# Optimization experiments

Measured on AMD Instinct MI355X. Metric: run time of the kernel, lower is better.

Reference implementation:

```python
import jax, jax.numpy as jnp
import numpy as np

H_PATCH = 32
W_PATCH = 32
DIM = 512
HEADS = 8
DIM_HEAD = 64
INNER = HEADS * DIM_HEAD
N = H_PATCH * W_PATCH
BATCH = 32


def make_relative_position_index(h, w):
    coords = np.stack(np.meshgrid(np.arange(h), np.arange(w), indexing='ij'))  # [2,h,w]
    flat = coords.reshape(2, -1)  # [2, N]
    rel = flat[:, :, None] - flat[:, None, :]  # [2, N, N]
    rel = rel.transpose(1, 2, 0).copy()  # [N, N, 2]
    rel[:, :, 0] += h - 1
    rel[:, :, 1] += w - 1
    rel[:, :, 0] *= 2 * h - 1
    return jnp.asarray(rel.sum(-1), dtype=jnp.int32)  # [N, N]


def setup_inputs() -> dict:
    key = jax.random.key(0)
    k1, k2, k3, k4 = jax.random.split(key, 4)
    x = jax.random.normal(k1, (BATCH, N, DIM), dtype=jnp.float32)
    w_qkv = jax.random.normal(k2, (DIM, 3 * INNER), dtype=jnp.float32) * (DIM ** -0.5)
    w_out = jax.random.normal(k3, (INNER, DIM), dtype=jnp.float32) * (INNER ** -0.5)
    b_out = jnp.zeros((DIM,), dtype=jnp.float32)
    bias_table = jax.random.normal(k4, ((2 * H_PATCH - 1) * (2 * W_PATCH - 1), HEADS), dtype=jnp.float32) * 0.02
    rel_index = make_relative_position_index(H_PATCH, W_PATCH)
    return {"x": x, "w_qkv": w_qkv, "w_out": w_out, "b_out": b_out,
            "bias_table": bias_table, "rel_index": rel_index}


def reference(x, w_qkv, w_out, b_out, bias_table, rel_index):
    b, n, _ = x.shape
    scale = DIM_HEAD ** -0.5
    qkv = x @ w_qkv  # [b, n, 3*inner]
    q, k, v = jnp.split(qkv, 3, axis=-1)
    def heads(t):
        return t.reshape(b, n, HEADS, DIM_HEAD).transpose(0, 2, 1, 3)  # [b,h,n,d]
    q, k, v = heads(q), heads(k), heads(v)
    dots = jnp.einsum('bhnd,bhmd->bhnm', q, k) * scale  # [b,h,n,n]
    bias = bias_table[rel_index]  # [n,n,heads]
    dots = dots + bias.transpose(2, 0, 1)[None]  # [b,h,n,n]
    attn = jax.nn.softmax(dots, axis=-1)
    out = jnp.einsum('bhnm,bhmd->bhnd', attn, v)
    out = out.transpose(0, 2, 1, 3).reshape(b, n, INNER)
    return out @ w_out + b_out
```

## Files before the change

### kernel.cpp

```cpp
#include <hip/hip_runtime.h>
#include <stdint.h>

typedef unsigned short u16;
typedef __attribute__((ext_vector_type(8))) short short8;
typedef __attribute__((ext_vector_type(4))) float floatx4;

__device__ __forceinline__ u16 f2bf(float f) {
  union { float f; unsigned u; } v; v.f = f;
  return (u16)((v.u + 0x7FFFu + ((v.u >> 16) & 1u)) >> 16);
}
__device__ __forceinline__ void gl_lds16(const void* g, void* l) {
  __builtin_amdgcn_global_load_lds((const __attribute__((address_space(1))) void*)g,
                                   (__attribute__((address_space(3))) void*)l, 16, 0, 0);
}
__device__ __forceinline__ float exp2_fast(float x) {
#if __has_builtin(__builtin_amdgcn_exp2f)
  return __builtin_amdgcn_exp2f(x);
#else
  return exp2f(x);
#endif
}

__global__ __launch_bounds__(256) void k_cast_x(const float* __restrict__ x, u16* __restrict__ xb) {
  int t = blockIdx.x * 256 + threadIdx.x;
  const float4* xv = (const float4*)x;
  float4 a = xv[2 * t], b = xv[2 * t + 1];
  short8 o;
  o[0] = f2bf(a.x); o[1] = f2bf(a.y); o[2] = f2bf(a.z); o[3] = f2bf(a.w);
  o[4] = f2bf(b.x); o[5] = f2bf(b.y); o[6] = f2bf(b.z); o[7] = f2bf(b.w);
  ((short8*)xb)[t] = o;
}

__global__ __launch_bounds__(256) void k_prep_w(const float* __restrict__ wqkv, const float* __restrict__ wout,
                                                u16* __restrict__ wqkvT, u16* __restrict__ woutT) {
  int t = blockIdx.x * 256 + threadIdx.x;
  if (t < 786432) {
    int n = t >> 9, k = t & 511;
    wqkvT[t] = f2bf(wqkv[k * 1536 + n]);
  } else {
    int u = t - 786432;
    int n = u >> 9, k = u & 511;
    woutT[u] = f2bf(wout[k * 512 + n]);
  }
}

__global__ __launch_bounds__(256) void k_prep_bias(const int* __restrict__ rel, const float* __restrict__ tab,
                                                   u16* __restrict__ biasb) {
  int t = blockIdx.x * 256 + threadIdx.x;
  int r    = t & 3;
  int ti   = (t >> 2) & 1;
  int l15  = (t >> 3) & 15;
  int quad = (t >> 7) & 3;
  int w    = (t >> 9) & 3;
  int kt   = (t >> 11) & 7;
  int qt   = (t >> 14) & 7;
  int h    = t >> 17;
  int qrow = qt * 128 + w * 32 + ti * 16 + quad * 4 + r;
  const int* rr = rel + qrow * 1024 + kt * 128 + l15;
  short8 o;
  #pragma unroll
  for (int tj = 0; tj < 8; tj++) {
    int idx = rr[tj * 16];
    o[tj] = f2bf((tab[idx * 8 + h] - 8.0f) * 1.44269504f);
  }
  ((short8*)biasb)[t] = o;
}

__global__ __launch_bounds__(256) void k_gemm_qkv(const u16* __restrict__ xb, const u16* __restrict__ wT,
                                                  u16* __restrict__ qbuf, u16* __restrict__ kbuf,
                                                  u16* __restrict__ vtbuf) {
  __shared__ u16 sm[17408];
  const int bn = blockIdx.x, bm = blockIdx.y;
  const int tid = threadIdx.x, w = tid >> 6, lane = tid & 63;
  const int quad = lane >> 4, l15 = lane & 15;
  const int wr = w >> 1, wc = w & 1;
  const u16* Ag = xb + (size_t)bm * 128 * 512;
  const u16* Bg = wT + (size_t)bn * 128 * 512;
  floatx4 acc[4][4];
  floatx4 zero = {0.f, 0.f, 0.f, 0.f};
  #pragma unroll
  for (int i = 0; i < 4; i++)
    #pragma unroll
    for (int j = 0; j < 4; j++) acc[i][j] = zero;

  for (int kb = 0; kb < 512; kb += 32) {
    __syncthreads();
    #pragma unroll
    for (int i = 0; i < 2; i++) {
      int c = w * 128 + i * 64 + lane;
      int row = c >> 2, col = (c & 3) * 8;
      gl_lds16(Ag + (size_t)row * 512 + kb + col, &sm[(w * 128 + i * 64) * 8]);
      gl_lds16(Bg + (size_t)row * 512 + kb + col, &sm[4096 + (w * 128 + i * 64) * 8]);
    }
    __syncthreads();
    short8 af[4], bf[4];
    #pragma unroll
    for (int ti = 0; ti < 4; ti++)
      af[ti] = *(const short8*)&sm[(wr * 64 + ti * 16 + l15) * 32 + quad * 8];
    #pragma unroll
    for (int tj = 0; tj < 4; tj++)
      bf[tj] = *(const short8*)&sm[4096 + (wc * 64 + tj * 16 + l15) * 32 + quad * 8];
    #pragma unroll
    for (int ti = 0; ti < 4; ti++)
      #pragma unroll
      for (int tj = 0; tj < 4; tj++)
        acc[ti][tj] = __builtin_amdgcn_mfma_f32_16x16x32_bf16(af[ti], bf[tj], acc[ti][tj], 0, 0, 0);
  }
  __syncthreads();
  #pragma unroll
  for (int ti = 0; ti < 4; ti++)
    #pragma unroll
    for (int tj = 0; tj < 4; tj++)
      #pragma unroll
      for (int r = 0; r < 4; r++)
        sm[(wr * 64 + ti * 16 + quad * 4 + r) * 136 + wc * 64 + tj * 16 + l15] = f2bf(acc[ti][tj][r]);
  __syncthreads();
  const int b = bm >> 3;
  const int nrow0 = (bm & 7) * 128;
  if (bn < 8) {
    u16* dst = (bn < 4) ? qbuf : kbuf;
    #pragma unroll
    for (int i = 0; i < 8; i++) {
      int chunk = i * 256 + tid;
      int r = chunk >> 4, c8 = chunk & 15;
      int nin = (bn & 3) * 128 + c8 * 8;
      int h = nin >> 6, d = nin & 63;
      uint4 val = *(const uint4*)&sm[r * 136 + c8 * 8];
      *(uint4*)&dst[(((size_t)(b * 8 + h)) * 1024 + nrow0 + r) * 64 + d] = val;
    }
  } else {
    #pragma unroll
    for (int i = 0; i < 8; i++) {
      int chunk = i * 256 + tid;
      int dcol = chunk & 127, nr8 = chunk >> 7;
      int nin = (bn & 3) * 128 + dcol;
      int h = nin >> 6, d = nin & 63;
      short8 v;
      #pragma unroll
      for (int j = 0; j < 8; j++) v[j] = (short)sm[(nr8 * 8 + j) * 136 + dcol];
      *(short8*)&vtbuf[(((size_t)(b * 8 + h)) * 64 + d) * 1024 + nrow0 + nr8 * 8] = v;
    }
  }
}

__global__ __launch_bounds__(256, 2) void k_attn(const u16* __restrict__ qbuf, const u16* __restrict__ kbuf,
                                                 const u16* __restrict__ vtbuf, const u16* __restrict__ biasb,
                                                 u16* __restrict__ attn_out) {
  __shared__ u16 sm[40960];
  const int PO = 32768;
  const int b = blockIdx.x, h = blockIdx.y >> 3, qt = blockIdx.y & 7;
  const int tid = threadIdx.x, w = tid >> 6, lane = tid & 63;
  const int quad = lane >> 4, l15 = lane & 15;
  const int xm = l15 & 7;
  u16* pw = &sm[PO + w * 2048];
  const size_t bh = (size_t)(b * 8 + h);
  const u16* qg = qbuf + (bh * 1024 + (size_t)qt * 128) * 64;
  const u16* kg = kbuf + bh * 1024 * 64;
  const u16* vg = vtbuf + bh * 64 * 1024;
  const u16* bg = biasb + (size_t)h * 1048576 + (size_t)qt * 131072 +
                  (size_t)w * 4096 + quad * 1024 + l15 * 64;

  int rK[4], cK[4], dV[4], cV[4];
  #pragma unroll
  for (int i = 0; i < 4; i++) {
    int p = (w * 4 + i) * 64 + lane;
    rK[i] = p >> 3;  cK[i] = (p & 7) ^ (rK[i] & 7);
    dV[i] = p >> 4;  cV[i] = (p & 15) ^ (dV[i] & 7);
  }

  short8 qf[2][2];
  #pragma unroll
  for (int ti = 0; ti < 2; ti++)
    #pragma unroll
    for (int kk = 0; kk < 2; kk++)
      qf[ti][kk] = *(const short8*)&qg[(w * 32 + ti * 16 + l15) * 64 + kk * 32 + quad * 8];

  floatx4 oacc[2][4];
  floatx4 zero = {0.f, 0.f, 0.f, 0.f};
  #pragma unroll
  for (int i = 0; i < 2; i++)
    #pragma unroll
    for (int j = 0; j < 4; j++) oacc[i][j] = zero;
  float lrow[2][4];
  #pragma unroll
  for (int i = 0; i < 2; i++)
    #pragma unroll
    for (int r = 0; r < 4; r++) lrow[i][r] = 0.f;

  const float SC = 0.125f * 1.44269504f;

  #pragma unroll
  for (int i = 0; i < 4; i++) {
    gl_lds16(kg + (size_t)rK[i] * 64 + cK[i] * 8, &sm[(w * 4 + i) * 512]);
    gl_lds16(vg + (size_t)dV[i] * 1024 + cV[i] * 8, &sm[8192 + (w * 4 + i) * 512]);
  }
  __syncthreads();

  for (int kt = 0; kt < 8; kt++) {
    const int cur = (kt & 1) ? 16384 : 0;
    const int nxt = (kt & 1) ? 0 : 16384;
    if (kt < 7) {
      #pragma unroll
      for (int i = 0; i < 4; i++) {
        gl_lds16(kg + (size_t)((kt + 1) * 128 + rK[i]) * 64 + cK[i] * 8, &sm[nxt + (w * 4 + i) * 512]);
        gl_lds16(vg + (size_t)dV[i] * 1024 + (kt + 1) * 128 + cV[i] * 8, &sm[nxt + 8192 + (w * 4 + i) * 512]);
      }
    }
    const u16* bkt = bg + kt * 16384;
    uint2 bu[2][4][2];
    #pragma unroll
    for (int ti = 0; ti < 2; ti++)
      #pragma unroll
      for (int r = 0; r < 4; r++) {
        bu[ti][r][0] = *(const uint2*)&bkt[(ti * 4 + r) * 8];
        bu[ti][r][1] = *(const uint2*)&bkt[(ti * 4 + r) * 8 + 4];
      }

    #pragma unroll
    for (int tjh = 0; tjh < 2; tjh++) {
      floatx4 sacc[2][4];
      #pragma unroll
      for (int tjl = 0; tjl < 4; tjl++) { sacc[0][tjl] = zero; sacc[1][tjl] = zero; }
      #pragma unroll
      for (int tjl = 0; tjl < 4; tjl++) {
        int tj = tjh * 4 + tjl;
        #pragma unroll
        for (int kk = 0; kk < 2; kk++) {
          short8 kf = *(const short8*)&sm[cur + (tj * 16 + l15) * 64 + ((kk * 4 + quad) ^ xm) * 8];
          sacc[0][tjl] = __builtin_amdgcn_mfma_f32_16x16x32_bf16(qf[0][kk], kf, sacc[0][tjl], 0, 0, 0);
          sacc[1][tjl] = __builtin_amdgcn_mfma_f32_16x16x32_bf16(qf[1][kk], kf, sacc[1][tjl], 0, 0, 0);
        }
      }
      #pragma unroll
      for (int ti = 0; ti < 2; ti++)
        #pragma unroll
        for (int r = 0; r < 4; r++) {
          int lr = ti * 16 + quad * 4 + r;
          int wm = lr & 7;
          unsigned blo = bu[ti][r][tjh].x, bhi = bu[ti][r][tjh].y;
          float bf32[4];
          bf32[0] = __builtin_bit_cast(float, blo << 16);
          bf32[1] = __builtin_bit_cast(float, blo & 0xFFFF0000u);
          bf32[2] = __builtin_bit_cast(float, bhi << 16);
          bf32[3] = __builtin_bit_cast(float, bhi & 0xFFFF0000u);
          float rs = 0.f;
          #pragma unroll
          for (int tjl = 0; tjl < 4; tjl++) {
            float p = exp2_fast(sacc[ti][tjl][r] * SC + bf32[tjl]);
            rs += p;
            unsigned pu = __builtin_bit_cast(unsigned, p);
            int cc = (tjl * 2 + (l15 >> 3)) ^ wm;
            pw[lr * 64 + cc * 8 + xm] = (u16)((pu + 0x8000u) >> 16);
          }
          lrow[ti][r] += rs;
        }
      #pragma unroll
      for (int kbl = 0; kbl < 2; kbl++) {
        short8 pf0 = *(const short8*)&pw[l15 * 64 + ((kbl * 4 + quad) ^ xm) * 8];
        short8 pf1 = *(const short8*)&pw[(16 + l15) * 64 + ((kbl * 4 + quad) ^ xm) * 8];
        #pragma unroll
        for (int dj = 0; dj < 4; dj++) {
          int kc = (tjh * 8 + kbl * 4 + quad) ^ xm;
          short8 vf = *(const short8*)&sm[cur + 8192 + (dj * 16 + l15) * 128 + kc * 8];
          oacc[0][dj] = __builtin_amdgcn_mfma_f32_16x16x32_bf16(pf0, vf, oacc[0][dj], 0, 0, 0);
          oacc[1][dj] = __builtin_amdgcn_mfma_f32_16x16x32_bf16(pf1, vf, oacc[1][dj], 0, 0, 0);
        }
      }
    }
    __syncthreads();
  }

  #pragma unroll
  for (int ti = 0; ti < 2; ti++)
    #pragma unroll
    for (int r = 0; r < 4; r++) {
      float s = lrow[ti][r];
      s += __shfl_xor(s, 1); s += __shfl_xor(s, 2);
      s += __shfl_xor(s, 4); s += __shfl_xor(s, 8);
      float inv = 1.f / s;
      int row = w * 32 + ti * 16 + quad * 4 + r;
      size_t ob = ((size_t)(b * 1024 + qt * 128 + row)) * 512 + h * 64;
      #pragma unroll
      for (int dj = 0; dj < 4; dj++)
        attn_out[ob + dj * 16 + l15] = f2bf(oacc[ti][dj][r] * inv);
    }
}

__global__ __launch_bounds__(256) void k_gemm_out(const u16* __restrict__ ab, const u16* __restrict__ wT,
                                                  const float* __restrict__ bout, float* __restrict__ out) {
  __shared__ u16 sm[8192];
  const int bn = blockIdx.x, bm = blockIdx.y;
  const int tid = threadIdx.x, w = tid >> 6, lane = tid & 63;
  const int quad = lane >> 4, l15 = lane & 15;
  const int wr = w >> 1, wc = w & 1;
  const u16* Ag = ab + (size_t)bm * 128 * 512;
  const u16* Bg = wT + (size_t)bn * 128 * 512;
  float bv[4];
  #pragma unroll
  for (int tj = 0; tj < 4; tj++) bv[tj] = bout[bn * 128 + wc * 64 + tj * 16 + l15];
  floatx4 acc[4][4];
  floatx4 zero = {0.f, 0.f, 0.f, 0.f};
  #pragma unroll
  for (int i = 0; i < 4; i++)
    #pragma unroll
    for (int j = 0; j < 4; j++) acc[i][j] = zero;

  for (int kb = 0; kb < 512; kb += 32) {
    __syncthreads();
    #pragma unroll
    for (int i = 0; i < 2; i++) {
      int c = w * 128 + i * 64 + lane;
      int row = c >> 2, col = (c & 3) * 8;
      gl_lds16(Ag + (size_t)row * 512 + kb + col, &sm[(w * 128 + i * 64) * 8]);
      gl_lds16(Bg + (size_t)row * 512 + kb + col, &sm[4096 + (w * 128 + i * 64) * 8]);
    }
    __syncthreads();
    short8 af[4], bf[4];
    #pragma unroll
    for (int ti = 0; ti < 4; ti++)
      af[ti] = *(const short8*)&sm[(wr * 64 + ti * 16 + l15) * 32 + quad * 8];
    #pragma unroll
    for (int tj = 0; tj < 4; tj++)
      bf[tj] = *(const short8*)&sm[4096 + (wc * 64 + tj * 16 + l15) * 32 + quad * 8];
    #pragma unroll
    for (int ti = 0; ti < 4; ti++)
      #pragma unroll
      for (int tj = 0; tj < 4; tj++)
        acc[ti][tj] = __builtin_amdgcn_mfma_f32_16x16x32_bf16(af[ti], bf[tj], acc[ti][tj], 0, 0, 0);
  }
  #pragma unroll
  for (int ti = 0; ti < 4; ti++)
    #pragma unroll
    for (int tj = 0; tj < 4; tj++)
      #pragma unroll
      for (int r = 0; r < 4; r++) {
        int row = bm * 128 + wr * 64 + ti * 16 + quad * 4 + r;
        int colg = bn * 128 + wc * 64 + tj * 16 + l15;
        out[(size_t)row * 512 + colg] = acc[ti][tj][r] + bv[tj];
      }
}

extern "C" void kernel_launch(void* const* d_in, const int* in_sizes, int n_in,
                              void* d_out, int out_size, void* d_ws, size_t ws_size,
                              hipStream_t stream) {
  const float* x    = (const float*)d_in[0];
  const float* wqkv = (const float*)d_in[1];
  const float* wout = (const float*)d_in[2];
  const float* bout = (const float*)d_in[3];
  const float* btab = (const float*)d_in[4];
  const int*   rel  = (const int*)d_in[5];
  char* ws = (char*)d_ws;
  u16* xb    = (u16*)(ws + 0);
  u16* qbuf  = (u16*)(ws + 33554432);
  u16* kbuf  = (u16*)(ws + 67108864);
  u16* vtbuf = (u16*)(ws + 100663296);
  u16* biasb = (u16*)(ws + 134217728);
  u16* wqkvT = (u16*)(ws + 150994944);
  u16* woutT = (u16*)(ws + 152567808);
  float* out = (float*)d_out;

  k_cast_x  <<<8192, 256, 0, stream>>>(x, xb);
  k_prep_w  <<<4096, 256, 0, stream>>>(wqkv, wout, wqkvT, woutT);
  k_prep_bias<<<4096, 256, 0, stream>>>(rel, btab, biasb);
  k_gemm_qkv<<<dim3(12, 256), 256, 0, stream>>>(xb, wqkvT, qbuf, kbuf, vtbuf);
  k_attn    <<<dim3(32, 64), 256, 0, stream>>>(qbuf, kbuf, vtbuf, biasb, xb);
  k_gemm_out<<<dim3(4, 256), 256, 0, stream>>>(xb, woutT, bout, out);
}
```

Before: 389.4 us.

## Halve attention KV tile to 64 keys to raise occupancy to three blocks

Shrinks each double-buffered K/V tile in the attention kernel from 128 to 64 keys, cutting shared memory from 80KB to 48KB per block and raising launch bounds to 3 blocks per CU. The loop now runs 16 iterations of 64 keys with a flatter body and V layout rows of 64. The aim is more resident waves to hide load and exp latency, at the cost of twice as many barriers and tighter register budgets that could cause spills.

```diff
diff --git a/kernel.cpp b/kernel.cpp
--- a/kernel.cpp
+++ b/kernel.cpp
@@ -143,11 +143,11 @@
   }
 }
 
-__global__ __launch_bounds__(256, 2) void k_attn(const u16* __restrict__ qbuf, const u16* __restrict__ kbuf,
+__global__ __launch_bounds__(256, 3) void k_attn(const u16* __restrict__ qbuf, const u16* __restrict__ kbuf,
                                                  const u16* __restrict__ vtbuf, const u16* __restrict__ biasb,
                                                  u16* __restrict__ attn_out) {
-  __shared__ u16 sm[40960];
-  const int PO = 32768;
+  __shared__ u16 sm[24576];
+  const int PO = 16384;
   const int b = blockIdx.x, h = blockIdx.y >> 3, qt = blockIdx.y & 7;
   const int tid = threadIdx.x, w = tid >> 6, lane = tid & 63;
   const int quad = lane >> 4, l15 = lane & 15;
@@ -160,12 +160,11 @@
   const u16* bg = biasb + (size_t)h * 1048576 + (size_t)qt * 131072 +
                   (size_t)w * 4096 + quad * 1024 + l15 * 64;
 
-  int rK[4], cK[4], dV[4], cV[4];
-  #pragma unroll
-  for (int i = 0; i < 4; i++) {
-    int p = (w * 4 + i) * 64 + lane;
-    rK[i] = p >> 3;  cK[i] = (p & 7) ^ (rK[i] & 7);
-    dV[i] = p >> 4;  cV[i] = (p & 15) ^ (dV[i] & 7);
+  int rS[2], cS[2];
+  #pragma unroll
+  for (int i = 0; i < 2; i++) {
+    int p = (w * 2 + i) * 64 + lane;
+    rS[i] = p >> 3;  cS[i] = (p & 7) ^ (rS[i] & 7);
   }
 
   short8 qf[2][2];
@@ -190,81 +189,78 @@
   const float SC = 0.125f * 1.44269504f;
 
   #pragma unroll
-  for (int i = 0; i < 4; i++) {
-    gl_lds16(kg + (size_t)rK[i] * 64 + cK[i] * 8, &sm[(w * 4 + i) * 512]);
-    gl_lds16(vg + (size_t)dV[i] * 1024 + cV[i] * 8, &sm[8192 + (w * 4 + i) * 512]);
+  for (int i = 0; i < 2; i++) {
+    gl_lds16(kg + (size_t)rS[i] * 64 + cS[i] * 8, &sm[(w * 2 + i) * 512]);
+    gl_lds16(vg + (size_t)rS[i] * 1024 + cS[i] * 8, &sm[4096 + (w * 2 + i) * 512]);
   }
   __syncthreads();
 
-  for (int kt = 0; kt < 8; kt++) {
-    const int cur = (kt & 1) ? 16384 : 0;
-    const int nxt = (kt & 1) ? 0 : 16384;
-    if (kt < 7) {
-      #pragma unroll
-      for (int i = 0; i < 4; i++) {
-        gl_lds16(kg + (size_t)((kt + 1) * 128 + rK[i]) * 64 + cK[i] * 8, &sm[nxt + (w * 4 + i) * 512]);
-        gl_lds16(vg + (size_t)dV[i] * 1024 + (kt + 1) * 128 + cV[i] * 8, &sm[nxt + 8192 + (w * 4 + i) * 512]);
-      }
-    }
-    const u16* bkt = bg + kt * 16384;
-    uint2 bu[2][4][2];
+  for (int kt = 0; kt < 16; kt++) {
+    const int cur = (kt & 1) ? 8192 : 0;
+    const int nxt = (kt & 1) ? 0 : 8192;
+    if (kt < 15) {
+      const int kn = (kt + 1) * 64;
+      #pragma unroll
+      for (int i = 0; i < 2; i++) {
+        gl_lds16(kg + (size_t)(kn + rS[i]) * 64 + cS[i] * 8, &sm[nxt + (w * 2 + i) * 512]);
+        gl_lds16(vg + (size_t)rS[i] * 1024 + kn + cS[i] * 8, &sm[nxt + 4096 + (w * 2 + i) * 512]);
+      }
+    }
+    const u16* bkt = bg + (kt >> 1) * 16384;
+    const int hf = (kt & 1) * 4;
+    uint2 bu[2][4];
     #pragma unroll
     for (int ti = 0; ti < 2; ti++)
       #pragma unroll
+      for (int r = 0; r < 4; r++)
+        bu[ti][r] = *(const uint2*)&bkt[(ti * 4 + r) * 8 + hf];
+
+    floatx4 sacc[2][4];
+    #pragma unroll
+    for (int tjl = 0; tjl < 4; tjl++) { sacc[0][tjl] = zero; sacc[1][tjl] = zero; }
+    #pragma unroll
+    for (int tjl = 0; tjl < 4; tjl++)
+      #pragma unroll
+      for (int kk = 0; kk < 2; kk++) {
+        short8 kf = *(const short8*)&sm[cur + (tjl * 16 + l15) * 64 + ((kk * 4 + quad) ^ xm) * 8];
+        sacc[0][tjl] = __builtin_amdgcn_mfma_f32_16x16x32_bf16(qf[0][kk], kf, sacc[0][tjl], 0, 0, 0);
+        sacc[1][tjl] = __builtin_amdgcn_mfma_f32_16x16x32_bf16(qf[1][kk], kf, sacc[1][tjl], 0, 0, 0);
+      }
+
+    #pragma unroll
+    for (int ti = 0; ti < 2; ti++)
+      #pragma unroll
       for (int r = 0; r < 4; r++) {
-        bu[ti][r][0] = *(const uint2*)&bkt[(ti * 4 + r) * 8];
-        bu[ti][r][1] = *(const uint2*)&bkt[(ti * 4 + r) * 8 + 4];
-      }
-
-    #pragma unroll
-    for (int tjh = 0; tjh < 2; tjh++) {
-      floatx4 sacc[2][4];
-      #pragma unroll
-      for (int tjl = 0; tjl < 4; tjl++) { sacc[0][tjl] = zero; sacc[1][tjl] = zero; }
-      #pragma unroll
-      for (int tjl = 0; tjl < 4; tjl++) {
-        int tj = tjh * 4 + tjl;
+        int lr = ti * 16 + quad * 4 + r;
+        int wm = lr & 7;
+        unsigned blo = bu[ti][r].x, bhi = bu[ti][r].y;
+        float bf32[4];
+        bf32[0] = __builtin_bit_cast(float, blo << 16);
+        bf32[1] = __builtin_bit_cast(float, blo & 0xFFFF0000u);
+        bf32[2] = __builtin_bit_cast(float, bhi << 16);
+        bf32[3] = __builtin_bit_cast(float, bhi & 0xFFFF0000u);
+        float rs = 0.f;
         #pragma unroll
-        for (int kk = 0; kk < 2; kk++) {
-          short8 kf = *(const short8*)&sm[cur + (tj * 16 + l15) * 64 + ((kk * 4 + quad) ^ xm) * 8];
-          sacc[0][tjl] = __builtin_amdgcn_mfma_f32_16x16x32_bf16(qf[0][kk], kf, sacc[0][tjl], 0, 0, 0);
-          sacc[1][tjl] = __builtin_amdgcn_mfma_f32_16x16x32_bf16(qf[1][kk], kf, sacc[1][tjl], 0, 0, 0);
+        for (int tjl = 0; tjl < 4; tjl++) {
+          float p = exp2_fast(sacc[ti][tjl][r] * SC + bf32[tjl]);
+          rs += p;
+          unsigned pu = __builtin_bit_cast(unsigned, p);
+          int cc = (tjl * 2 + (l15 >> 3)) ^ wm;
+          pw[lr * 64 + cc * 8 + xm] = (u16)((pu + 0x8000u) >> 16);
         }
-      }
-      #pragma unroll
-      for (int ti = 0; ti < 2; ti++)
-        #pragma unroll
-        for (int r = 0; r < 4; r++) {
-          int lr = ti * 16 + quad * 4 + r;
-          int wm = lr & 7;
-          unsigned blo = bu[ti][r][tjh].x, bhi = bu[ti][r][tjh].y;
-          float bf32[4];
-          bf32[0] = __builtin_bit_cast(float, blo << 16);
-          bf32[1] = __builtin_bit_cast(float, blo & 0xFFFF0000u);
-          bf32[2] = __builtin_bit_cast(float, bhi << 16);
-          bf32[3] = __builtin_bit_cast(float, bhi & 0xFFFF0000u);
-          float rs = 0.f;
-          #pragma unroll
-          for (int tjl = 0; tjl < 4; tjl++) {
-            float p = exp2_fast(sacc[ti][tjl][r] * SC + bf32[tjl]);
-            rs += p;
-            unsigned pu = __builtin_bit_cast(unsigned, p);
-            int cc = (tjl * 2 + (l15 >> 3)) ^ wm;
-            pw[lr * 64 + cc * 8 + xm] = (u16)((pu + 0x8000u) >> 16);
-          }
-          lrow[ti][r] += rs;
-        }
-      #pragma unroll
-      for (int kbl = 0; kbl < 2; kbl++) {
-        short8 pf0 = *(const short8*)&pw[l15 * 64 + ((kbl * 4 + quad) ^ xm) * 8];
-        short8 pf1 = *(const short8*)&pw[(16 + l15) * 64 + ((kbl * 4 + quad) ^ xm) * 8];
-        #pragma unroll
-        for (int dj = 0; dj < 4; dj++) {
-          int kc = (tjh * 8 + kbl * 4 + quad) ^ xm;
-          short8 vf = *(const short8*)&sm[cur + 8192 + (dj * 16 + l15) * 128 + kc * 8];
-          oacc[0][dj] = __builtin_amdgcn_mfma_f32_16x16x32_bf16(pf0, vf, oacc[0][dj], 0, 0, 0);
-          oacc[1][dj] = __builtin_amdgcn_mfma_f32_16x16x32_bf16(pf1, vf, oacc[1][dj], 0, 0, 0);
-        }
+        lrow[ti][r] += rs;
+      }
+
+    #pragma unroll
+    for (int kbl = 0; kbl < 2; kbl++) {
+      const int gsl = ((kbl * 4 + quad) ^ xm) * 8;
+      short8 pf0 = *(const short8*)&pw[l15 * 64 + gsl];
+      short8 pf1 = *(const short8*)&pw[(16 + l15) * 64 + gsl];
+      #pragma unroll
+      for (int dj = 0; dj < 4; dj++) {
+        short8 vf = *(const short8*)&sm[cur + 4096 + (dj * 16 + l15) * 64 + gsl];
+        oacc[0][dj] = __builtin_amdgcn_mfma_f32_16x16x32_bf16(pf0, vf, oacc[0][dj], 0, 0, 0);
+        oacc[1][dj] = __builtin_amdgcn_mfma_f32_16x16x32_bf16(pf1, vf, oacc[1][dj], 0, 0, 0);
       }
     }
     __syncthreads();
```

New measurement: 421.5 us. 8.2% more time.

## Transpose QK^T MFMA so each lane owns a query row, vectorize P stores

Applied to the files above, without the earlier changes.

Swaps the MFMA operand order for the score computation so each lane holds four consecutive key columns of one query row. This lets the probabilities be written to LDS as 4-element vector stores instead of scalar 16-bit stores, and the row sums collapse to two per lane with a cheaper cross-lane reduction. The precomputed bias layout and its prep kernel are reworked to match, so bias is loaded as 16-byte vectors per half-tile. The normalisation now needs an extra shuffle to bring each row's inverse back to the output layout, and the probability rounding switches to round-to-nearest-even via f2bf.

```diff
diff --git a/kernel.cpp b/kernel.cpp
--- a/kernel.cpp
+++ b/kernel.cpp
@@ -3,6 +3,7 @@
 
 typedef unsigned short u16;
 typedef __attribute__((ext_vector_type(8))) short short8;
+typedef __attribute__((ext_vector_type(4))) short s16x4;
 typedef __attribute__((ext_vector_type(4))) float floatx4;
 
 __device__ __forceinline__ u16 f2bf(float f) {
@@ -47,21 +48,25 @@
 __global__ __launch_bounds__(256) void k_prep_bias(const int* __restrict__ rel, const float* __restrict__ tab,
                                                    u16* __restrict__ biasb) {
   int t = blockIdx.x * 256 + threadIdx.x;
-  int r    = t & 3;
-  int ti   = (t >> 2) & 1;
-  int l15  = (t >> 3) & 15;
-  int quad = (t >> 7) & 3;
-  int w    = (t >> 9) & 3;
-  int kt   = (t >> 11) & 7;
+  int half = t & 1;
+  int lane = (t >> 1) & 63;
+  int ti   = (t >> 7) & 1;
+  int w    = (t >> 8) & 3;
+  int kt   = (t >> 10) & 15;
   int qt   = (t >> 14) & 7;
   int h    = t >> 17;
-  int qrow = qt * 128 + w * 32 + ti * 16 + quad * 4 + r;
-  const int* rr = rel + qrow * 1024 + kt * 128 + l15;
+  int l15 = lane & 15, quad = lane >> 4;
+  int qrow = qt * 128 + w * 32 + ti * 16 + l15;
+  const int* rr = rel + (size_t)qrow * 1024 + kt * 64 + quad * 4;
   short8 o;
   #pragma unroll
-  for (int tj = 0; tj < 8; tj++) {
-    int idx = rr[tj * 16];
-    o[tj] = f2bf((tab[idx * 8 + h] - 8.0f) * 1.44269504f);
+  for (int j = 0; j < 2; j++) {
+    int tjl = half * 2 + j;
+    int4 idx = *(const int4*)&rr[tjl * 16];
+    o[j * 4 + 0] = f2bf((tab[idx.x * 8 + h] - 8.0f) * 1.44269504f);
+    o[j * 4 + 1] = f2bf((tab[idx.y * 8 + h] - 8.0f) * 1.44269504f);
+    o[j * 4 + 2] = f2bf((tab[idx.z * 8 + h] - 8.0f) * 1.44269504f);
+    o[j * 4 + 3] = f2bf((tab[idx.w * 8 + h] - 8.0f) * 1.44269504f);
   }
   ((short8*)biasb)[t] = o;
 }
@@ -152,13 +157,13 @@
   const int tid = threadIdx.x, w = tid >> 6, lane = tid & 63;
   const int quad = lane >> 4, l15 = lane & 15;
   const int xm = l15 & 7;
+  const int qh = quad >> 1, ql = quad & 1;
   u16* pw = &sm[PO + w * 2048];
   const size_t bh = (size_t)(b * 8 + h);
   const u16* qg = qbuf + (bh * 1024 + (size_t)qt * 128) * 64;
   const u16* kg = kbuf + bh * 1024 * 64;
   const u16* vg = vtbuf + bh * 64 * 1024;
-  const u16* bg = biasb + (size_t)h * 1048576 + (size_t)qt * 131072 +
-                  (size_t)w * 4096 + quad * 1024 + l15 * 64;
+  const u16* bg = biasb + (size_t)(h * 8 + qt) * 131072 + w * 2048 + lane * 16;
 
   int rK[4], cK[4], dV[4], cV[4];
   #pragma unroll
@@ -181,11 +186,7 @@
   for (int i = 0; i < 2; i++)
     #pragma unroll
     for (int j = 0; j < 4; j++) oacc[i][j] = zero;
-  float lrow[2][4];
-  #pragma unroll
-  for (int i = 0; i < 2; i++)
-    #pragma unroll
-    for (int r = 0; r < 4; r++) lrow[i][r] = 0.f;
+  float lrow[2] = {0.f, 0.f};
 
   const float SC = 0.125f * 1.44269504f;
 
@@ -206,58 +207,58 @@
         gl_lds16(vg + (size_t)dV[i] * 1024 + (kt + 1) * 128 + cV[i] * 8, &sm[nxt + 8192 + (w * 4 + i) * 512]);
       }
     }
-    const u16* bkt = bg + kt * 16384;
-    uint2 bu[2][4][2];
-    #pragma unroll
-    for (int ti = 0; ti < 2; ti++)
-      #pragma unroll
-      for (int r = 0; r < 4; r++) {
-        bu[ti][r][0] = *(const uint2*)&bkt[(ti * 4 + r) * 8];
-        bu[ti][r][1] = *(const uint2*)&bkt[(ti * 4 + r) * 8 + 4];
-      }
 
     #pragma unroll
     for (int tjh = 0; tjh < 2; tjh++) {
+      const u16* bkt = bg + (kt * 2 + tjh) * 8192;
+      const uint4 bA0 = *(const uint4*)&bkt[0];
+      const uint4 bB0 = *(const uint4*)&bkt[8];
+      const uint4 bA1 = *(const uint4*)&bkt[1024];
+      const uint4 bB1 = *(const uint4*)&bkt[1024 + 8];
+
       floatx4 sacc[2][4];
       #pragma unroll
       for (int tjl = 0; tjl < 4; tjl++) { sacc[0][tjl] = zero; sacc[1][tjl] = zero; }
       #pragma unroll
-      for (int tjl = 0; tjl < 4; tjl++) {
-        int tj = tjh * 4 + tjl;
+      for (int tjl = 0; tjl < 4; tjl++)
         #pragma unroll
         for (int kk = 0; kk < 2; kk++) {
-          short8 kf = *(const short8*)&sm[cur + (tj * 16 + l15) * 64 + ((kk * 4 + quad) ^ xm) * 8];
-          sacc[0][tjl] = __builtin_amdgcn_mfma_f32_16x16x32_bf16(qf[0][kk], kf, sacc[0][tjl], 0, 0, 0);
-          sacc[1][tjl] = __builtin_amdgcn_mfma_f32_16x16x32_bf16(qf[1][kk], kf, sacc[1][tjl], 0, 0, 0);
+          short8 kf = *(const short8*)&sm[cur + (tjh * 64 + tjl * 16 + l15) * 64 + ((kk * 4 + quad) ^ xm) * 8];
+          sacc[0][tjl] = __builtin_amdgcn_mfma_f32_16x16x32_bf16(kf, qf[0][kk], sacc[0][tjl], 0, 0, 0);
+          sacc[1][tjl] = __builtin_amdgcn_mfma_f32_16x16x32_bf16(kf, qf[1][kk], sacc[1][tjl], 0, 0, 0);
+        }
+
+      #pragma unroll
+      for (int ti = 0; ti < 2; ti++) {
+        const uint4 bA = ti ? bA1 : bA0;
+        const uint4 bB = ti ? bB1 : bB0;
+        const int prow = (ti * 16 + l15) * 64;
+        #pragma unroll
+        for (int tjl = 0; tjl < 4; tjl++) {
+          unsigned ulo = (tjl == 0) ? bA.x : (tjl == 1) ? bA.z : (tjl == 2) ? bB.x : bB.z;
+          unsigned uhi = (tjl == 0) ? bA.y : (tjl == 1) ? bA.w : (tjl == 2) ? bB.y : bB.w;
+          float b0 = __builtin_bit_cast(float, ulo << 16);
+          float b1 = __builtin_bit_cast(float, ulo & 0xFFFF0000u);
+          float b2 = __builtin_bit_cast(float, uhi << 16);
+          float b3 = __builtin_bit_cast(float, uhi & 0xFFFF0000u);
+          float p0 = exp2_fast(sacc[ti][tjl][0] * SC + b0);
+          float p1 = exp2_fast(sacc[ti][tjl][1] * SC + b1);
+          float p2 = exp2_fast(sacc[ti][tjl][2] * SC + b2);
+          float p3 = exp2_fast(sacc[ti][tjl][3] * SC + b3);
+          lrow[ti] += (p0 + p1) + (p2 + p3);
+          s16x4 pv;
+          pv[0] = (short)f2bf(p0); pv[1] = (short)f2bf(p1);
+          pv[2] = (short)f2bf(p2); pv[3] = (short)f2bf(p3);
+          *(s16x4*)&pw[prow + ((tjl * 2 + qh) ^ xm) * 8 + ql * 4] = pv;
         }
       }
-      #pragma unroll
-      for (int ti = 0; ti < 2; ti++)
-        #pragma unroll
-        for (int r = 0; r < 4; r++) {
-          int lr = ti * 16 + quad * 4 + r;
-          int wm = lr & 7;
-          unsigned blo = bu[ti][r][tjh].x, bhi = bu[ti][r][tjh].y;
-          float bf32[4];
-          bf32[0] = __builtin_bit_cast(float, blo << 16);
-          bf32[1] = __builtin_bit_cast(float, blo & 0xFFFF0000u);
-          bf32[2] = __builtin_bit_cast(float, bhi << 16);
-          bf32[3] = __builtin_bit_cast(float, bhi & 0xFFFF0000u);
-          float rs = 0.f;
-          #pragma unroll
-          for (int tjl = 0; tjl < 4; tjl++) {
-            float p = exp2_fast(sacc[ti][tjl][r] * SC + bf32[tjl]);
-            rs += p;
-            unsigned pu = __builtin_bit_cast(unsigned, p);
-            int cc = (tjl * 2 + (l15 >> 3)) ^ wm;
-            pw[lr * 64 + cc * 8 + xm] = (u16)((pu + 0x8000u) >> 16);
-          }
-          lrow[ti][r] += rs;
-        }
+      asm volatile("" ::: "memory");
+
       #pragma unroll
       for (int kbl = 0; kbl < 2; kbl++) {
-        short8 pf0 = *(const short8*)&pw[l15 * 64 + ((kbl * 4 + quad) ^ xm) * 8];
-        short8 pf1 = *(const short8*)&pw[(16 + l15) * 64 + ((kbl * 4 + quad) ^ xm) * 8];
+        const int gslP = ((kbl * 4 + quad) ^ xm) * 8;
+        short8 pf0 = *(const short8*)&pw[l15 * 64 + gslP];
+        short8 pf1 = *(const short8*)&pw[(16 + l15) * 64 + gslP];
         #pragma unroll
         for (int dj = 0; dj < 4; dj++) {
           int kc = (tjh * 8 + kbl * 4 + quad) ^ xm;
@@ -271,19 +272,21 @@
   }
 
   #pragma unroll
-  for (int ti = 0; ti < 2; ti++)
+  for (int ti = 0; ti < 2; ti++) {
+    float s = lrow[ti];
+    s += __shfl_xor(s, 16);
+    s += __shfl_xor(s, 32);
+    float inv = 1.f / s;
     #pragma unroll
     for (int r = 0; r < 4; r++) {
-      float s = lrow[ti][r];
-      s += __shfl_xor(s, 1); s += __shfl_xor(s, 2);
-      s += __shfl_xor(s, 4); s += __shfl_xor(s, 8);
-      float inv = 1.f / s;
+      float invr = __shfl(inv, (lane & 48) | (quad * 4 + r));
       int row = w * 32 + ti * 16 + quad * 4 + r;
       size_t ob = ((size_t)(b * 1024 + qt * 128 + row)) * 512 + h * 64;
       #pragma unroll
       for (int dj = 0; dj < 4; dj++)
-        attn_out[ob + dj * 16 + l15] = f2bf(oacc[ti][dj][r] * inv);
-    }
+        attn_out[ob + dj * 16 + l15] = f2bf(oacc[ti][dj][r] * invr);
+    }
+  }
 }
 
 __global__ __launch_bounds__(256) void k_gemm_out(const u16* __restrict__ ab, const u16* __restrict__ wT,
```

Result: faster. 375.1 us (-3.7%).
